# Kernel tuning notes

Measured on AMD Instinct MI355X. Metric: run time of the kernel, lower is better.

## Reference

```python
import jax, jax.numpy as jnp
import numpy as np

N_USER, N_MOVIE = 100000, 20000
D_USER, D_MOVIE = 32, 64
H = 64
E = 2000000
B = 200000


def _sage(x_src, x_dst, src, dst, W_l, b_l, W_r, n_dst):
    # PyG SAGEConv: out = lin_l(mean_{j in N(i)} x_j) + lin_r(x_i)
    msg = x_src[src]                                   # [E, d_src] gather
    agg = jax.ops.segment_sum(msg, dst, num_segments=n_dst)
    cnt = jax.ops.segment_sum(jnp.ones((src.shape[0],), x_src.dtype), dst,
                              num_segments=n_dst)
    mean = agg / jnp.maximum(cnt, 1.0)[:, None]        # [n_dst, d_src]
    return mean @ W_l + b_l + x_dst @ W_r


def setup_inputs() -> dict:
    key = jax.random.key(0)
    ks = jax.random.split(key, 24)
    f = jnp.float32

    def lin(k, din, dout):
        s = 1.0 / np.sqrt(din)
        return jax.random.uniform(k, (din, dout), f, -s, s)

    inp = {
        'x_user': jax.random.normal(ks[0], (N_USER, D_USER), f),
        'x_movie': jax.random.normal(ks[1], (N_MOVIE, D_MOVIE), f),
        'src_um': jax.random.randint(ks[2], (E,), 0, N_USER),
        'dst_um': jax.random.randint(ks[3], (E,), 0, N_MOVIE),
        'src_mu': jax.random.randint(ks[4], (E,), 0, N_MOVIE),
        'dst_mu': jax.random.randint(ks[5], (E,), 0, N_USER),
        'label_row': jax.random.randint(ks[6], (B,), 0, N_USER),
        'label_col': jax.random.randint(ks[7], (B,), 0, N_MOVIE),
        # layer 1, edge type user->movie (dst=movie): lin_l on aggregated src (user feats)
        'W1_um_l': lin(ks[8], D_USER, H), 'b1_um': jnp.zeros((H,), f),
        'W1_um_r': lin(ks[9], D_MOVIE, H),
        # layer 1, edge type movie->user (dst=user)
        'W1_mu_l': lin(ks[10], D_MOVIE, H), 'b1_mu': jnp.zeros((H,), f),
        'W1_mu_r': lin(ks[11], D_USER, H),
        # layer 2 (inputs are hidden H for both types)
        'W2_um_l': lin(ks[12], H, H), 'b2_um': jnp.zeros((H,), f),
        'W2_um_r': lin(ks[13], H, H),
        'W2_mu_l': lin(ks[14], H, H), 'b2_mu': jnp.zeros((H,), f),
        'W2_mu_r': lin(ks[15], H, H),
        # head: Linear(2H, 2)
        'W_lin': lin(ks[16], 2 * H, 2), 'b_lin': jnp.zeros((2,), f),
    }
    return inp


def reference(x_user, x_movie, src_um, dst_um, src_mu, dst_mu,
              label_row, label_col,
              W1_um_l, b1_um, W1_um_r, W1_mu_l, b1_mu, W1_mu_r,
              W2_um_l, b2_um, W2_um_r, W2_mu_l, b2_mu, W2_mu_r,
              W_lin, b_lin):
    # layer 1 (to_hetero aggr='sum': each node type has one incoming edge type)
    h_movie = _sage(x_user, x_movie, src_um, dst_um, W1_um_l, b1_um, W1_um_r, N_MOVIE)
    h_user = _sage(x_movie, x_user, src_mu, dst_mu, W1_mu_l, b1_mu, W1_mu_r, N_USER)
    h_movie = jax.nn.relu(h_movie)
    h_user = jax.nn.relu(h_user)
    # layer 2
    z_movie = _sage(h_user, h_movie, src_um, dst_um, W2_um_l, b2_um, W2_um_r, N_MOVIE)
    z_user = _sage(h_movie, h_user, src_mu, dst_mu, W2_mu_l, b2_mu, W2_mu_r, N_USER)
    # head
    concat = jnp.concatenate([z_user[label_row], z_movie[label_col]], axis=-1)
    out = concat @ W_lin + b_lin                       # [B, 2]
    mu = out[:, 0]
    sigma = jax.nn.softplus(out[:, 1]) + 1e-6
    return mu, sigma
```

## Files before the change

kernel.cpp:

```cpp
#include <hip/hip_runtime.h>
#include <hip/hip_bf16.h>
#include <hip/hip_fp16.h>
#include <type_traits>

#define NB_UM 157
#define NB_MU 196
#define NBALL 353
#define NBLK 256

using f16x8 = __attribute__((ext_vector_type(8))) _Float16;
using f32x4 = __attribute__((ext_vector_type(4))) float;


__global__ __launch_bounds__(256) void cast_half2(const float* __restrict__ a,
                                                  __half* __restrict__ ah, int na,
                                                  const float* __restrict__ b,
                                                  __half* __restrict__ bh, int nb) {
    int i = blockIdx.x * blockDim.x + threadIdx.x;
    int st = gridDim.x * blockDim.x;
    for (int k = i; k < na / 2; k += st) {
        float2 v = ((const float2*)a)[k];
        ((__half2*)ah)[k] = __floats2half2_rn(v.x, v.y);
    }
    for (int k = i; k < nb / 2; k += st) {
        float2 v = ((const float2*)b)[k];
        ((__half2*)bh)[k] = __floats2half2_rn(v.x, v.y);
    }
}


__global__ __launch_bounds__(1024) void hist_part(const int* __restrict__ dst_um,
                                                  const int* __restrict__ dst_mu,
                                                  int* __restrict__ histM, int E, int chunk) {
    __shared__ int h[NBALL];
    for (int i = threadIdx.x; i < NBALL; i += 1024) h[i] = 0;
    __syncthreads();
    int blk = blockIdx.x;
    int s = blk * chunk, e = min(E, s + chunk);
    if (s < e) {
        int n4 = (e - s) >> 2;
        const int4* du4 = (const int4*)(dst_um + s);
        const int4* dm4 = (const int4*)(dst_mu + s);
        for (int i = threadIdx.x; i < n4; i += 1024) {
            int4 d = du4[i];
            atomicAdd(&h[d.x >> 7], 1);
            atomicAdd(&h[d.y >> 7], 1);
            atomicAdd(&h[d.z >> 7], 1);
            atomicAdd(&h[d.w >> 7], 1);
            int4 m = dm4[i];
            atomicAdd(&h[NB_UM + (m.x >> 9)], 1);
            atomicAdd(&h[NB_UM + (m.y >> 9)], 1);
            atomicAdd(&h[NB_UM + (m.z >> 9)], 1);
            atomicAdd(&h[NB_UM + (m.w >> 9)], 1);
        }
        for (int i = s + (n4 << 2) + threadIdx.x; i < e; i += 1024) {
            atomicAdd(&h[dst_um[i] >> 7], 1);
            atomicAdd(&h[NB_UM + (dst_mu[i] >> 9)], 1);
        }
    }
    __syncthreads();
    for (int i = threadIdx.x; i < NBALL; i += 1024) histM[i * NBLK + blk] = h[i];
}


__global__ __launch_bounds__(256) void bucket_totals(int* __restrict__ histM,
                                                     int* __restrict__ btot, int nball) {
    int w = (blockIdx.x * blockDim.x + threadIdx.x) >> 6;
    int lane = threadIdx.x & 63;
    if (w >= nball) return;
    int* row = histM + w * NBLK;
    int v[4];
    int s = 0;
#pragma unroll
    for (int i = 0; i < 4; i++) {
        int c = row[lane * 4 + i];
        v[i] = s;
        s += c;
    }
    int incl = s;
    for (int d = 1; d < 64; d <<= 1) {
        int y = __shfl_up(incl, d, 64);
        if (lane >= d) incl += y;
    }
    int excl = incl - s;
#pragma unroll
    for (int i = 0; i < 4; i++) row[lane * 4 + i] = excl + v[i];
    if (lane == 63) btot[w] = incl;
}


__global__ __launch_bounds__(256) void boff_scan(const int* __restrict__ btot,
                                                 int* __restrict__ boff, int nball,
                                                 int* __restrict__ off_um, int NM,
                                                 int* __restrict__ off_mu, int NU, int E) {
    __shared__ int sdata[256];
    int t = threadIdx.x;
    int v[8];
    int sum = 0;
#pragma unroll
    for (int i = 0; i < 8; i++) {
        int idx = t * 8 + i;
        int c = (idx < nball) ? btot[idx] : 0;
        v[i] = sum;
        sum += c;
    }
    sdata[t] = sum;
    __syncthreads();
    for (int s = 1; s < 256; s <<= 1) {
        int y = (t >= s) ? sdata[t - s] : 0;
        __syncthreads();
        sdata[t] += y;
        __syncthreads();
    }
    int base = (t == 0) ? 0 : sdata[t - 1];
#pragma unroll
    for (int i = 0; i < 8; i++) {
        int idx = t * 8 + i;
        if (idx < nball) boff[idx] = base + v[i];
    }
    if (t == 0) {
        boff[nball] = 2 * E;
        off_um[NM] = E;
        off_mu[NU] = E;
    }
}


__global__ __launch_bounds__(1024) void partition2(const int* __restrict__ src_um,
                                                   const int* __restrict__ dst_um,
                                                   const int* __restrict__ src_mu,
                                                   const int* __restrict__ dst_mu,
                                                   const int* __restrict__ histM,
                                                   const int* __restrict__ boff,
                                                   int* __restrict__ tmp, int E, int chunk) {
    __shared__ int cur[NBALL];
    int blk = blockIdx.x;
    for (int i = threadIdx.x; i < NBALL; i += 1024)
        cur[i] = histM[i * NBLK + blk] + boff[i];
    __syncthreads();
    int s = blk * chunk, e = min(E, s + chunk);
    if (s >= e) return;
    int n4 = (e - s) >> 2;
    const int4* su4 = (const int4*)(src_um + s);
    const int4* du4 = (const int4*)(dst_um + s);
    const int4* sm4 = (const int4*)(src_mu + s);
    const int4* dm4 = (const int4*)(dst_mu + s);
    for (int i = threadIdx.x; i < n4; i += 1024) {
        int4 sv = su4[i];
        int4 dv = du4[i];
        int p;
        p = atomicAdd(&cur[dv.x >> 7], 1); tmp[p] = sv.x | ((dv.x & 127) << 20);
        p = atomicAdd(&cur[dv.y >> 7], 1); tmp[p] = sv.y | ((dv.y & 127) << 20);
        p = atomicAdd(&cur[dv.z >> 7], 1); tmp[p] = sv.z | ((dv.z & 127) << 20);
        p = atomicAdd(&cur[dv.w >> 7], 1); tmp[p] = sv.w | ((dv.w & 127) << 20);
        int4 sv2 = sm4[i];
        int4 dv2 = dm4[i];
        p = atomicAdd(&cur[NB_UM + (dv2.x >> 9)], 1); tmp[p] = sv2.x | ((dv2.x & 511) << 20);
        p = atomicAdd(&cur[NB_UM + (dv2.y >> 9)], 1); tmp[p] = sv2.y | ((dv2.y & 511) << 20);
        p = atomicAdd(&cur[NB_UM + (dv2.z >> 9)], 1); tmp[p] = sv2.z | ((dv2.z & 511) << 20);
        p = atomicAdd(&cur[NB_UM + (dv2.w >> 9)], 1); tmp[p] = sv2.w | ((dv2.w & 511) << 20);
    }
    for (int i = s + (n4 << 2) + threadIdx.x; i < e; i += 1024) {
        int d = dst_um[i];
        int p = atomicAdd(&cur[d >> 7], 1);
        tmp[p] = src_um[i] | ((d & 127) << 20);
        int d2 = dst_mu[i];
        int q = atomicAdd(&cur[NB_UM + (d2 >> 9)], 1);
        tmp[q] = src_mu[i] | ((d2 & 511) << 20);
    }
}


__global__ __launch_bounds__(1024) void scatter_both(const int* __restrict__ tmp,
                                                     const int* __restrict__ boff,
                                                     int* __restrict__ off_um,
                                                     int* __restrict__ csr_um, int NM,
                                                     int* __restrict__ off_mu,
                                                     int* __restrict__ csr_mu, int NU, int E) {
    __shared__ int lcnt[512];
    __shared__ int lcur[512];
    __shared__ int sdata[1024];
    int b = blockIdx.x;
    int um = (b < NB_UM);
    int W = um ? 128 : 512;
    int n = um ? NM : NU;
    int sub = um ? 0 : E;
    int* off = um ? off_um : off_mu;
    int* csr = um ? csr_um : csr_mu;
    int rowbase = (um ? b : (b - NB_UM)) * W;
    int t = threadIdx.x;
    int s = boff[b], e = boff[b + 1];
    for (int j = t; j < W; j += 1024) lcnt[j] = 0;
    __syncthreads();
    for (int i = s + t; i < e; i += 1024) atomicAdd(&lcnt[tmp[i] >> 20], 1);
    __syncthreads();
    int myc = (t < W) ? lcnt[t] : 0;
    sdata[t] = myc;
    __syncthreads();
    for (int d = 1; d < 1024; d <<= 1) {
        int y = (t >= d) ? sdata[t - d] : 0;
        __syncthreads();
        sdata[t] += y;
        __syncthreads();
    }
    if (t < W) lcur[t] = s + sdata[t] - myc;
    __syncthreads();
    for (int j = t; j < W; j += 1024)
        if (rowbase + j < n) off[rowbase + j] = lcur[j] - sub;
    __syncthreads();
    for (int i = s + t; i < e; i += 1024) {
        int vv = tmp[i];
        int p = atomicAdd(&lcur[vv >> 20], 1);
        csr[p - sub] = vv & 0xFFFFF;
    }
}


__device__ __forceinline__ void acc8(float* a, uint4 r) {
    const __half2* h = reinterpret_cast<const __half2*>(&r);
#pragma unroll
    for (int j = 0; j < 4; j++) {
        float2 f = __half22float2(h[j]);
        a[2 * j] += f.x;
        a[2 * j + 1] += f.y;
    }
}

template <int D>
__global__ __launch_bounds__(256) void agg_mean_g(const int* __restrict__ csr,
                                                  const int* __restrict__ off,
                                                  const __half* __restrict__ xh,
                                                  float* __restrict__ out, int nrows) {
    constexpr int L = D / 8;
    int gid = (blockIdx.x * blockDim.x + threadIdx.x) / L;
    int lg = threadIdx.x & (L - 1);
    int ngroups = (gridDim.x * blockDim.x) / L;
    int c8 = lg * 8;
    for (int row = gid; row < nrows; row += ngroups) {
        int s = off[row], e = off[row + 1];
        float a[8] = {0.f, 0.f, 0.f, 0.f, 0.f, 0.f, 0.f, 0.f};
        int k = s;
        for (; k + 4 <= e; k += 4) {
            int i0 = csr[k], i1 = csr[k + 1], i2 = csr[k + 2], i3 = csr[k + 3];
            uint4 r0 = *(const uint4*)&xh[(long)i0 * D + c8];
            uint4 r1 = *(const uint4*)&xh[(long)i1 * D + c8];
            uint4 r2 = *(const uint4*)&xh[(long)i2 * D + c8];
            uint4 r3 = *(const uint4*)&xh[(long)i3 * D + c8];
            acc8(a, r0); acc8(a, r1); acc8(a, r2); acc8(a, r3);
        }
        for (; k < e; ++k) {
            uint4 r0 = *(const uint4*)&xh[(long)csr[k] * D + c8];
            acc8(a, r0);
        }
        float inv = 1.0f / fmaxf((float)(e - s), 1.0f);
        float4 q0 = make_float4(a[0] * inv, a[1] * inv, a[2] * inv, a[3] * inv);
        float4 q1 = make_float4(a[4] * inv, a[5] * inv, a[6] * inv, a[7] * inv);
        *(float4*)&out[(long)row * D + c8] = q0;
        *(float4*)&out[(long)row * D + c8 + 4] = q1;
    }
}


template <int Dm, int Dd, bool RELU, typename TX, typename TO>
__global__ __launch_bounds__(256) void dense_mfma(const float* __restrict__ mean,
                                                  const TX* __restrict__ xd,
                                                  const float* __restrict__ Wl,
                                                  const float* __restrict__ Wr,
                                                  const float* __restrict__ bias,
                                                  TO* __restrict__ out, int n) {
    constexpr int K = Dm + Dd;
    constexpr int SAP = K + 8;
    __shared__ __align__(16) _Float16 sA[64 * SAP];
    __shared__ __align__(16) _Float16 sWt[64 * SAP];
    __shared__ float sb[64];
    int t = threadIdx.x;
    int R0 = blockIdx.x * 64;

    for (int i = t; i < K * 16; i += 256) {
        int k = i >> 4, c = (i & 15) * 4;
        float4 v = (k < Dm) ? *(const float4*)&Wl[k * 64 + c]
                            : *(const float4*)&Wr[(k - Dm) * 64 + c];
        sWt[(c + 0) * SAP + k] = (_Float16)v.x;
        sWt[(c + 1) * SAP + k] = (_Float16)v.y;
        sWt[(c + 2) * SAP + k] = (_Float16)v.z;
        sWt[(c + 3) * SAP + k] = (_Float16)v.w;
    }
    if (t < 64) sb[t] = bias[t];
    constexpr int QR = K / 4;
    for (int i = t; i < 64 * QR; i += 256) {
        int r = i / QR, c = (i % QR) * 4;
        int gr = R0 + r;
        float4 v = make_float4(0.f, 0.f, 0.f, 0.f);
        if (gr < n) {
            if (c < Dm) {
                v = *(const float4*)&mean[(long)gr * Dm + c];
            } else {
                if constexpr (std::is_same<TX, __half>::value) {
                    const __half* p = &xd[(long)gr * Dd + (c - Dm)];
                    v = make_float4(__half2float(p[0]), __half2float(p[1]),
                                    __half2float(p[2]), __half2float(p[3]));
                } else {
                    v = *(const float4*)&xd[(long)gr * Dd + (c - Dm)];
                }
            }
        }
        _Float16* p = &sA[r * SAP + c];
        p[0] = (_Float16)v.x; p[1] = (_Float16)v.y;
        p[2] = (_Float16)v.z; p[3] = (_Float16)v.w;
    }
    __syncthreads();

    int w = t >> 6, lane = t & 63;
    int lr = lane & 15, lg = lane >> 4;
    f32x4 acc[4];
#pragma unroll
    for (int nt = 0; nt < 4; nt++) {
        float bb = sb[16 * nt + lr];
        acc[nt][0] = bb; acc[nt][1] = bb; acc[nt][2] = bb; acc[nt][3] = bb;
    }
    int arow = 16 * w + lr;
#pragma unroll
    for (int kk = 0; kk < K / 32; kk++) {
        int k0 = kk * 32 + 8 * lg;
        f16x8 a = *(const f16x8*)&sA[arow * SAP + k0];
#pragma unroll
        for (int nt = 0; nt < 4; nt++) {
            f16x8 b = *(const f16x8*)&sWt[(16 * nt + lr) * SAP + k0];
            acc[nt] = __builtin_amdgcn_mfma_f32_16x16x32_f16(a, b, acc[nt], 0, 0, 0);
        }
    }
#pragma unroll
    for (int nt = 0; nt < 4; nt++) {
#pragma unroll
        for (int r = 0; r < 4; r++) {
            int gr = R0 + 16 * w + lg * 4 + r;
            if (gr >= n) continue;
            float vv = acc[nt][r];
            if (RELU) vv = fmaxf(vv, 0.f);
            int gc = 16 * nt + lr;
            if constexpr (std::is_same<TO, __half>::value) {
                out[(long)gr * 64 + gc] = __float2half(vv);
            } else {
                out[(long)gr * 64 + gc] = vv;
            }
        }
    }
}


__global__ __launch_bounds__(256) void proj_kernel(const float* __restrict__ z,
                                                   const float* __restrict__ Wlin,
                                                   int woff, const float* __restrict__ blin,
                                                   int addb, float2* __restrict__ p, int n) {
    __shared__ float sW0[64], sW1[64];
    int t = threadIdx.x;
    if (t < 64) {
        sW0[t] = Wlin[(woff + t) * 2 + 0];
        sW1[t] = Wlin[(woff + t) * 2 + 1];
    }
    __syncthreads();
    float b0 = addb ? blin[0] : 0.f;
    float b1 = addb ? blin[1] : 0.f;
    int lane = t & 63;
    int w = t >> 6;
    int lr = lane & 15, q = lane >> 4;
    int row = blockIdx.x * 16 + w * 4 + q;
    if (row >= n) return;
    float4 zv = *(const float4*)&z[(long)row * 64 + lr * 4];
    float p0 = zv.x * sW0[lr * 4] + zv.y * sW0[lr * 4 + 1] + zv.z * sW0[lr * 4 + 2] + zv.w * sW0[lr * 4 + 3];
    float p1 = zv.x * sW1[lr * 4] + zv.y * sW1[lr * 4 + 1] + zv.z * sW1[lr * 4 + 2] + zv.w * sW1[lr * 4 + 3];
#pragma unroll
    for (int m = 1; m < 16; m <<= 1) {
        p0 += __shfl_xor(p0, m, 64);
        p1 += __shfl_xor(p1, m, 64);
    }
    if (lr == 0) p[row] = make_float2(p0 + b0, p1 + b1);
}


__global__ __launch_bounds__(256) void head_gather(const float2* __restrict__ pu,
                                                   const float2* __restrict__ pm,
                                                   const int* __restrict__ lrow,
                                                   const int* __restrict__ lcol,
                                                   float* __restrict__ out, int B) {
    int i = blockIdx.x * blockDim.x + threadIdx.x;
    int st = gridDim.x * blockDim.x;
    for (int b = i; b < B; b += st) {
        float2 a = pu[lrow[b]];
        float2 d = pm[lcol[b]];
        float m = a.x + d.x;
        float x = a.y + d.y;
        float sp = fmaxf(x, 0.f) + log1pf(expf(-fabsf(x)));
        out[b] = m;
        out[B + b] = sp + 1e-6f;
    }
}


extern "C" void kernel_launch(void* const* d_in, const int* in_sizes, int n_in,
                              void* d_out, int out_size, void* d_ws, size_t ws_size,
                              hipStream_t stream) {
    const float* x_user  = (const float*)d_in[0];
    const float* x_movie = (const float*)d_in[1];
    const int* src_um = (const int*)d_in[2];
    const int* dst_um = (const int*)d_in[3];
    const int* src_mu = (const int*)d_in[4];
    const int* dst_mu = (const int*)d_in[5];
    const int* lrow = (const int*)d_in[6];
    const int* lcol = (const int*)d_in[7];
    const float* W1_um_l = (const float*)d_in[8];
    const float* b1_um   = (const float*)d_in[9];
    const float* W1_um_r = (const float*)d_in[10];
    const float* W1_mu_l = (const float*)d_in[11];
    const float* b1_mu   = (const float*)d_in[12];
    const float* W1_mu_r = (const float*)d_in[13];
    const float* W2_um_l = (const float*)d_in[14];
    const float* b2_um   = (const float*)d_in[15];
    const float* W2_um_r = (const float*)d_in[16];
    const float* W2_mu_l = (const float*)d_in[17];
    const float* b2_mu   = (const float*)d_in[18];
    const float* W2_mu_r = (const float*)d_in[19];
    const float* W_lin   = (const float*)d_in[20];
    const float* b_lin   = (const float*)d_in[21];
    float* out = (float*)d_out;

    const int E  = in_sizes[2];
    const int B  = in_sizes[6];
    const int NU = in_sizes[0] / 32;
    const int NM = in_sizes[1] / 64;

    char* wsp = (char*)d_ws;
    size_t o = 0;
    auto alloc = [&](size_t bytes) {
        size_t p = o;
        o += (bytes + 255) & ~(size_t)255;
        return (void*)(wsp + p);
    };
    int* off_um = (int*)alloc((size_t)(NM + 1) * 4);
    int* off_mu = (int*)alloc((size_t)(NU + 1) * 4);
    int* btot   = (int*)alloc((NBALL) * 4);
    int* boff   = (int*)alloc((NBALL + 1) * 4);
    int* csr_um = (int*)alloc((size_t)E * 4);
    int* csr_mu = (int*)alloc((size_t)E * 4);
    float* A_m  = (float*)alloc((size_t)NM * 64 * 4);
    float* A_u  = (float*)alloc((size_t)NU * 64 * 4);
    __half* Hh_m = (__half*)alloc((size_t)NM * 64 * 2);
    __half* Hh_u = (__half*)alloc((size_t)NU * 64 * 2);
    __half* xh_u = (__half*)alloc((size_t)NU * 32 * 2);
    __half* xh_m = (__half*)alloc((size_t)NM * 64 * 2);
    float2* pu  = (float2*)alloc((size_t)NU * 8);
    float2* pm  = (float2*)alloc((size_t)NM * 8);
    (void)ws_size;

    int* tmp   = (int*)A_u;
    int* histM = (int*)A_m;

    const int chunk = (((E + NBLK - 1) / NBLK) + 3) & ~3;

    cast_half2<<<512, 256, 0, stream>>>(x_user, xh_u, NU * 32, x_movie, xh_m, NM * 64);

    hist_part<<<NBLK, 1024, 0, stream>>>(dst_um, dst_mu, histM, E, chunk);
    bucket_totals<<<(NBALL + 3) / 4, 256, 0, stream>>>(histM, btot, NBALL);
    boff_scan<<<1, 256, 0, stream>>>(btot, boff, NBALL, off_um, NM, off_mu, NU, E);
    partition2<<<NBLK, 1024, 0, stream>>>(src_um, dst_um, src_mu, dst_mu, histM, boff,
                                          tmp, E, chunk);
    scatter_both<<<NBALL, 1024, 0, stream>>>(tmp, boff, off_um, csr_um, NM,
                                             off_mu, csr_mu, NU, E);

    agg_mean_g<32><<<(NM * 4 + 255) / 256, 256, 0, stream>>>(csr_um, off_um, xh_u, A_m, NM);
    dense_mfma<32, 64, true, float, __half><<<(NM + 63) / 64, 256, 0, stream>>>(
        A_m, x_movie, W1_um_l, W1_um_r, b1_um, Hh_m, NM);
    agg_mean_g<64><<<(NU * 8 + 255) / 256, 256, 0, stream>>>(csr_mu, off_mu, xh_m, A_u, NU);
    dense_mfma<64, 32, true, float, __half><<<(NU + 63) / 64, 256, 0, stream>>>(
        A_u, x_user, W1_mu_l, W1_mu_r, b1_mu, Hh_u, NU);

    agg_mean_g<64><<<(NM * 8 + 255) / 256, 256, 0, stream>>>(csr_um, off_um, Hh_u, A_m, NM);
    dense_mfma<64, 64, false, __half, float><<<(NM + 63) / 64, 256, 0, stream>>>(
        A_m, Hh_m, W2_um_l, W2_um_r, b2_um, A_m, NM);
    agg_mean_g<64><<<(NU * 8 + 255) / 256, 256, 0, stream>>>(csr_mu, off_mu, Hh_m, A_u, NU);
    dense_mfma<64, 64, false, __half, float><<<(NU + 63) / 64, 256, 0, stream>>>(
        A_u, Hh_u, W2_mu_l, W2_mu_r, b2_mu, A_u, NU);

    proj_kernel<<<(NU + 15) / 16, 256, 0, stream>>>(A_u, W_lin, 0, b_lin, 1, pu, NU);
    proj_kernel<<<(NM + 15) / 16, 256, 0, stream>>>(A_m, W_lin, 64, b_lin, 0, pm, NM);
    head_gather<<<1024, 256, 0, stream>>>(pu, pm, lrow, lcol, out, B);
}
```

Measured before the change: 262.2 us.

## Merge per-edge-type kernels into dual launches and widen CSR buckets

Pairs the user->movie and movie->user aggregation, dense MFMA and projection kernels into single launches that split the grid by block index. This cuts kernel count and lets the smaller movie-side work overlap with the user side. Bucket widths in the partition/scatter CSR build are doubled, halving the bucket count and doubling the per-block shared counters. The trade-off is fewer, larger scatter blocks, and dense blocks sized for the largest shared-memory variant.

After: 245.8 us. -6.2%, faster.

```diff
diff --git a/kernel.cpp b/kernel.cpp
--- a/kernel.cpp
+++ b/kernel.cpp
@@ -3,9 +3,9 @@
 #include <hip/hip_fp16.h>
 #include <type_traits>
 
-#define NB_UM 157
-#define NB_MU 196
-#define NBALL 353
+#define NB_UM 79
+#define NB_MU 98
+#define NBALL 177
 #define NBLK 256
 
 using f16x8 = __attribute__((ext_vector_type(8))) _Float16;
@@ -43,19 +43,19 @@
         const int4* dm4 = (const int4*)(dst_mu + s);
         for (int i = threadIdx.x; i < n4; i += 1024) {
             int4 d = du4[i];
-            atomicAdd(&h[d.x >> 7], 1);
-            atomicAdd(&h[d.y >> 7], 1);
-            atomicAdd(&h[d.z >> 7], 1);
-            atomicAdd(&h[d.w >> 7], 1);
+            atomicAdd(&h[d.x >> 8], 1);
+            atomicAdd(&h[d.y >> 8], 1);
+            atomicAdd(&h[d.z >> 8], 1);
+            atomicAdd(&h[d.w >> 8], 1);
             int4 m = dm4[i];
-            atomicAdd(&h[NB_UM + (m.x >> 9)], 1);
-            atomicAdd(&h[NB_UM + (m.y >> 9)], 1);
-            atomicAdd(&h[NB_UM + (m.z >> 9)], 1);
-            atomicAdd(&h[NB_UM + (m.w >> 9)], 1);
+            atomicAdd(&h[NB_UM + (m.x >> 10)], 1);
+            atomicAdd(&h[NB_UM + (m.y >> 10)], 1);
+            atomicAdd(&h[NB_UM + (m.z >> 10)], 1);
+            atomicAdd(&h[NB_UM + (m.w >> 10)], 1);
         }
         for (int i = s + (n4 << 2) + threadIdx.x; i < e; i += 1024) {
-            atomicAdd(&h[dst_um[i] >> 7], 1);
-            atomicAdd(&h[NB_UM + (dst_mu[i] >> 9)], 1);
+            atomicAdd(&h[dst_um[i] >> 8], 1);
+            atomicAdd(&h[NB_UM + (dst_mu[i] >> 10)], 1);
         }
     }
     __syncthreads();
@@ -149,24 +149,24 @@
         int4 sv = su4[i];
         int4 dv = du4[i];
         int p;
-        p = atomicAdd(&cur[dv.x >> 7], 1); tmp[p] = sv.x | ((dv.x & 127) << 20);
-        p = atomicAdd(&cur[dv.y >> 7], 1); tmp[p] = sv.y | ((dv.y & 127) << 20);
-        p = atomicAdd(&cur[dv.z >> 7], 1); tmp[p] = sv.z | ((dv.z & 127) << 20);
-        p = atomicAdd(&cur[dv.w >> 7], 1); tmp[p] = sv.w | ((dv.w & 127) << 20);
+        p = atomicAdd(&cur[dv.x >> 8], 1); tmp[p] = sv.x | ((dv.x & 255) << 20);
+        p = atomicAdd(&cur[dv.y >> 8], 1); tmp[p] = sv.y | ((dv.y & 255) << 20);
+        p = atomicAdd(&cur[dv.z >> 8], 1); tmp[p] = sv.z | ((dv.z & 255) << 20);
+        p = atomicAdd(&cur[dv.w >> 8], 1); tmp[p] = sv.w | ((dv.w & 255) << 20);
         int4 sv2 = sm4[i];
         int4 dv2 = dm4[i];
-        p = atomicAdd(&cur[NB_UM + (dv2.x >> 9)], 1); tmp[p] = sv2.x | ((dv2.x & 511) << 20);
-        p = atomicAdd(&cur[NB_UM + (dv2.y >> 9)], 1); tmp[p] = sv2.y | ((dv2.y & 511) << 20);
-        p = atomicAdd(&cur[NB_UM + (dv2.z >> 9)], 1); tmp[p] = sv2.z | ((dv2.z & 511) << 20);
-        p = atomicAdd(&cur[NB_UM + (dv2.w >> 9)], 1); tmp[p] = sv2.w | ((dv2.w & 511) << 20);
+        p = atomicAdd(&cur[NB_UM + (dv2.x >> 10)], 1); tmp[p] = sv2.x | ((dv2.x & 1023) << 20);
+        p = atomicAdd(&cur[NB_UM + (dv2.y >> 10)], 1); tmp[p] = sv2.y | ((dv2.y & 1023) << 20);
+        p = atomicAdd(&cur[NB_UM + (dv2.z >> 10)], 1); tmp[p] = sv2.z | ((dv2.z & 1023) << 20);
+        p = atomicAdd(&cur[NB_UM + (dv2.w >> 10)], 1); tmp[p] = sv2.w | ((dv2.w & 1023) << 20);
     }
     for (int i = s + (n4 << 2) + threadIdx.x; i < e; i += 1024) {
         int d = dst_um[i];
-        int p = atomicAdd(&cur[d >> 7], 1);
-        tmp[p] = src_um[i] | ((d & 127) << 20);
+        int p = atomicAdd(&cur[d >> 8], 1);
+        tmp[p] = src_um[i] | ((d & 255) << 20);
         int d2 = dst_mu[i];
-        int q = atomicAdd(&cur[NB_UM + (d2 >> 9)], 1);
-        tmp[q] = src_mu[i] | ((d2 & 511) << 20);
+        int q = atomicAdd(&cur[NB_UM + (d2 >> 10)], 1);
+        tmp[q] = src_mu[i] | ((d2 & 1023) << 20);
     }
 }
 
@@ -177,12 +177,12 @@
                                                      int* __restrict__ csr_um, int NM,
                                                      int* __restrict__ off_mu,
                                                      int* __restrict__ csr_mu, int NU, int E) {
-    __shared__ int lcnt[512];
-    __shared__ int lcur[512];
+    __shared__ int lcnt[1024];
+    __shared__ int lcur[1024];
     __shared__ int sdata[1024];
     int b = blockIdx.x;
     int um = (b < NB_UM);
-    int W = um ? 128 : 512;
+    int W = um ? 256 : 1024;
     int n = um ? NM : NU;
     int sub = um ? 0 : E;
     int* off = um ? off_um : off_mu;
@@ -227,14 +227,15 @@
 }
 
 template <int D>
-__global__ __launch_bounds__(256) void agg_mean_g(const int* __restrict__ csr,
-                                                  const int* __restrict__ off,
-                                                  const __half* __restrict__ xh,
-                                                  float* __restrict__ out, int nrows) {
+__device__ __forceinline__ void agg_body(const int* __restrict__ csr,
+                                         const int* __restrict__ off,
+                                         const __half* __restrict__ xh,
+                                         float* __restrict__ out, int nrows,
+                                         int bid, int nblocks) {
     constexpr int L = D / 8;
-    int gid = (blockIdx.x * blockDim.x + threadIdx.x) / L;
+    int gid = (bid * 256 + (int)threadIdx.x) / L;
     int lg = threadIdx.x & (L - 1);
-    int ngroups = (gridDim.x * blockDim.x) / L;
+    int ngroups = (nblocks * 256) / L;
     int c8 = lg * 8;
     for (int row = gid; row < nrows; row += ngroups) {
         int s = off[row], e = off[row + 1];
@@ -260,21 +261,50 @@
     }
 }
 
+__global__ __launch_bounds__(256) void agg_dual_l1(const int* __restrict__ csr_um,
+                                                   const int* __restrict__ off_um,
+                                                   const __half* __restrict__ xh_u,
+                                                   float* __restrict__ A_m, int NM, int g1,
+                                                   const int* __restrict__ csr_mu,
+                                                   const int* __restrict__ off_mu,
+                                                   const __half* __restrict__ xh_m,
+                                                   float* __restrict__ A_u, int NU) {
+    if ((int)blockIdx.x < g1)
+        agg_body<32>(csr_um, off_um, xh_u, A_m, NM, blockIdx.x, g1);
+    else
+        agg_body<64>(csr_mu, off_mu, xh_m, A_u, NU, blockIdx.x - g1, gridDim.x - g1);
+}
+
+__global__ __launch_bounds__(256) void agg_dual_l2(const int* __restrict__ csr_um,
+                                                   const int* __restrict__ off_um,
+                                                   const __half* __restrict__ Hh_u,
+                                                   float* __restrict__ A_m, int NM, int g1,
+                                                   const int* __restrict__ csr_mu,
+                                                   const int* __restrict__ off_mu,
+                                                   const __half* __restrict__ Hh_m,
+                                                   float* __restrict__ A_u, int NU) {
+    if ((int)blockIdx.x < g1)
+        agg_body<64>(csr_um, off_um, Hh_u, A_m, NM, blockIdx.x, g1);
+    else
+        agg_body<64>(csr_mu, off_mu, Hh_m, A_u, NU, blockIdx.x - g1, gridDim.x - g1);
+}
+
 
 template <int Dm, int Dd, bool RELU, typename TX, typename TO>
-__global__ __launch_bounds__(256) void dense_mfma(const float* __restrict__ mean,
-                                                  const TX* __restrict__ xd,
-                                                  const float* __restrict__ Wl,
-                                                  const float* __restrict__ Wr,
-                                                  const float* __restrict__ bias,
-                                                  TO* __restrict__ out, int n) {
+__device__ __forceinline__ void dense_body(char* smemraw,
+                                           const float* __restrict__ mean,
+                                           const TX* __restrict__ xd,
+                                           const float* __restrict__ Wl,
+                                           const float* __restrict__ Wr,
+                                           const float* __restrict__ bias,
+                                           TO* __restrict__ out, int n, int bid) {
     constexpr int K = Dm + Dd;
     constexpr int SAP = K + 8;
-    __shared__ __align__(16) _Float16 sA[64 * SAP];
-    __shared__ __align__(16) _Float16 sWt[64 * SAP];
-    __shared__ float sb[64];
+    _Float16* sA = (_Float16*)smemraw;
+    _Float16* sWt = sA + 64 * SAP;
+    float* sb = (float*)(sWt + 64 * SAP);
     int t = threadIdx.x;
-    int R0 = blockIdx.x * 64;
+    int R0 = bid * 64;
 
     for (int i = t; i < K * 16; i += 256) {
         int k = i >> 4, c = (i & 15) * 4;
@@ -347,11 +377,64 @@
     }
 }
 
-
-__global__ __launch_bounds__(256) void proj_kernel(const float* __restrict__ z,
-                                                   const float* __restrict__ Wlin,
-                                                   int woff, const float* __restrict__ blin,
-                                                   int addb, float2* __restrict__ p, int n) {
+#define DENSE_SMEM_BYTES (64 * 136 * 2 * 2 + 256)
+
+__global__ __launch_bounds__(256) void dense_dual_l1(const float* __restrict__ A_m,
+                                                     const float* __restrict__ x_movie,
+                                                     const float* __restrict__ W1l_um,
+                                                     const float* __restrict__ W1r_um,
+                                                     const float* __restrict__ b1_um,
+                                                     __half* __restrict__ Hh_m, int NM, int g1,
+                                                     const float* __restrict__ A_u,
+                                                     const float* __restrict__ x_user,
+                                                     const float* __restrict__ W1l_mu,
+                                                     const float* __restrict__ W1r_mu,
+                                                     const float* __restrict__ b1_mu,
+                                                     __half* __restrict__ Hh_u, int NU) {
+    __shared__ __align__(16) char smem[DENSE_SMEM_BYTES];
+    if ((int)blockIdx.x < g1)
+        dense_body<32, 64, true, float, __half>(smem, A_m, x_movie, W1l_um, W1r_um, b1_um,
+                                                Hh_m, NM, blockIdx.x);
+    else
+        dense_body<64, 32, true, float, __half>(smem, A_u, x_user, W1l_mu, W1r_mu, b1_mu,
+                                                Hh_u, NU, blockIdx.x - g1);
+}
+
+__global__ __launch_bounds__(256) void dense_dual_l2(float* __restrict__ A_m,
+                                                     const __half* __restrict__ Hh_m,
+                                                     const float* __restrict__ W2l_um,
+                                                     const float* __restrict__ W2r_um,
+                                                     const float* __restrict__ b2_um,
+                                                     int NM, int g1,
+                                                     float* __restrict__ A_u,
+                                                     const __half* __restrict__ Hh_u,
+                                                     const float* __restrict__ W2l_mu,
+                                                     const float* __restrict__ W2r_mu,
+                                                     const float* __restrict__ b2_mu,
+                                                     int NU) {
+    __shared__ __align__(16) char smem[DENSE_SMEM_BYTES];
+    if ((int)blockIdx.x < g1)
+        dense_body<64, 64, false, __half, float>(smem, A_m, Hh_m, W2l_um, W2r_um, b2_um,
+                                                 A_m, NM, blockIdx.x);
+    else
+        dense_body<64, 64, false, __half, float>(smem, A_u, Hh_u, W2l_mu, W2r_mu, b2_mu,
+                                                 A_u, NU, blockIdx.x - g1);
+}
+
+
+__global__ __launch_bounds__(256) void proj_dual(const float* __restrict__ zu,
+                                                 const float* __restrict__ zm,
+                                                 const float* __restrict__ Wlin,
+                                                 const float* __restrict__ blin,
+                                                 float2* __restrict__ pu,
+                                                 float2* __restrict__ pm,
+                                                 int NU, int NM, int gu) {
+    int isu = ((int)blockIdx.x < gu);
+    const float* z = isu ? zu : zm;
+    float2* p = isu ? pu : pm;
+    int n = isu ? NU : NM;
+    int woff = isu ? 0 : 64;
+    int bid = isu ? blockIdx.x : blockIdx.x - gu;
     __shared__ float sW0[64], sW1[64];
     int t = threadIdx.x;
     if (t < 64) {
@@ -359,12 +442,12 @@
         sW1[t] = Wlin[(woff + t) * 2 + 1];
     }
     __syncthreads();
-    float b0 = addb ? blin[0] : 0.f;
-    float b1 = addb ? blin[1] : 0.f;
+    float b0 = isu ? blin[0] : 0.f;
+    float b1 = isu ? blin[1] : 0.f;
     int lane = t & 63;
     int w = t >> 6;
     int lr = lane & 15, q = lane >> 4;
-    int row = blockIdx.x * 16 + w * 4 + q;
+    int row = bid * 16 + w * 4 + q;
     if (row >= n) return;
     float4 zv = *(const float4*)&z[(long)row * 64 + lr * 4];
     float p0 = zv.x * sW0[lr * 4] + zv.y * sW0[lr * 4 + 1] + zv.z * sW0[lr * 4 + 2] + zv.w * sW0[lr * 4 + 3];
@@ -467,21 +550,31 @@
     scatter_both<<<NBALL, 1024, 0, stream>>>(tmp, boff, off_um, csr_um, NM,
                                              off_mu, csr_mu, NU, E);
 
-    agg_mean_g<32><<<(NM * 4 + 255) / 256, 256, 0, stream>>>(csr_um, off_um, xh_u, A_m, NM);
-    dense_mfma<32, 64, true, float, __half><<<(NM + 63) / 64, 256, 0, stream>>>(
-        A_m, x_movie, W1_um_l, W1_um_r, b1_um, Hh_m, NM);
-    agg_mean_g<64><<<(NU * 8 + 255) / 256, 256, 0, stream>>>(csr_mu, off_mu, xh_m, A_u, NU);
-    dense_mfma<64, 32, true, float, __half><<<(NU + 63) / 64, 256, 0, stream>>>(
-        A_u, x_user, W1_mu_l, W1_mu_r, b1_mu, Hh_u, NU);
-
-    agg_mean_g<64><<<(NM * 8 + 255) / 256, 256, 0, stream>>>(csr_um, off_um, Hh_u, A_m, NM);
-    dense_mfma<64, 64, false, __half, float><<<(NM + 63) / 64, 256, 0, stream>>>(
-        A_m, Hh_m, W2_um_l, W2_um_r, b2_um, A_m, NM);
-    agg_mean_g<64><<<(NU * 8 + 255) / 256, 256, 0, stream>>>(csr_mu, off_mu, Hh_m, A_u, NU);
-    dense_mfma<64, 64, false, __half, float><<<(NU + 63) / 64, 256, 0, stream>>>(
-        A_u, Hh_u, W2_mu_l, W2_mu_r, b2_mu, A_u, NU);
-
-    proj_kernel<<<(NU + 15) / 16, 256, 0, stream>>>(A_u, W_lin, 0, b_lin, 1, pu, NU);
-    proj_kernel<<<(NM + 15) / 16, 256, 0, stream>>>(A_m, W_lin, 64, b_lin, 0, pm, NM);
+    {
+        int g1 = (NM * 4 + 255) / 256;
+        int g2 = (NU * 8 + 255) / 256;
+        agg_dual_l1<<<g1 + g2, 256, 0, stream>>>(csr_um, off_um, xh_u, A_m, NM, g1,
+                                                 csr_mu, off_mu, xh_m, A_u, NU);
+        int d1 = (NM + 63) / 64, d2 = (NU + 63) / 64;
+        dense_dual_l1<<<d1 + d2, 256, 0, stream>>>(A_m, x_movie, W1_um_l, W1_um_r, b1_um,
+                                                   Hh_m, NM, d1,
+                                                   A_u, x_user, W1_mu_l, W1_mu_r, b1_mu,
+                                                   Hh_u, NU);
+    }
+
+    {
+        int g1 = (NM * 8 + 255) / 256;
+        int g2 = (NU * 8 + 255) / 256;
+        agg_dual_l2<<<g1 + g2, 256, 0, stream>>>(csr_um, off_um, Hh_u, A_m, NM, g1,
+                                                 csr_mu, off_mu, Hh_m, A_u, NU);
+        int d1 = (NM + 63) / 64, d2 = (NU + 63) / 64;
+        dense_dual_l2<<<d1 + d2, 256, 0, stream>>>(A_m, Hh_m, W2_um_l, W2_um_r, b2_um, NM, d1,
+                                                   A_u, Hh_u, W2_mu_l, W2_mu_r, b2_mu, NU);
+    }
+
+    {
+        int gu = (NU + 15) / 16, gm = (NM + 15) / 16;
+        proj_dual<<<gu + gm, 256, 0, stream>>>(A_u, A_m, W_lin, b_lin, pu, pm, NU, NM, gu);
+    }
     head_gather<<<1024, 256, 0, stream>>>(pu, pm, lrow, lcol, out, B);
 }
```
